# Kernel optimization log

Hardware: AMD Instinct MI355X
Metric: run time of the kernel (lower is better)

Reference implementation:

```python
import jax, jax.numpy as jnp
import numpy as np

EMB_DIM = 512
R_DIM = 64
B, S = 8, 2048


def _lowrank_params(key):
    k1, k2, k3, k4 = jax.random.split(key, 4)
    s1 = 1.0 / np.sqrt(EMB_DIM)
    s2 = 1.0 / np.sqrt(R_DIM)
    w1 = jax.random.uniform(k1, (EMB_DIM, R_DIM), jnp.float32, -s1, s1)
    b1 = jax.random.uniform(k2, (R_DIM,), jnp.float32, -s1, s1)
    w2 = jax.random.uniform(k3, (R_DIM, EMB_DIM), jnp.float32, -s2, s2)
    b2 = jax.random.uniform(k4, (EMB_DIM,), jnp.float32, -s2, s2)
    return w1, b1, w2, b2


def setup_inputs() -> dict:
    key = jax.random.key(0)
    kx, km, kq, kk, kv = jax.random.split(key, 5)
    x = jax.random.normal(kx, (B, S, EMB_DIM), jnp.float32)
    attention_mask = jax.random.randint(km, (B, S), 0, 2, jnp.int32)
    q_w1, q_b1, q_w2, q_b2 = _lowrank_params(kq)
    k_w1, k_b1, k_w2, k_b2 = _lowrank_params(kk)
    v_w1, v_b1, v_w2, v_b2 = _lowrank_params(kv)
    return dict(x=x, attention_mask=attention_mask,
                q_w1=q_w1, q_b1=q_b1, q_w2=q_w2, q_b2=q_b2,
                k_w1=k_w1, k_b1=k_b1, k_w2=k_w2, k_b2=k_b2,
                v_w1=v_w1, v_b1=v_b1, v_w2=v_w2, v_b2=v_b2)


def _proj(x, w1, b1, w2, b2):
    # low-rank projection: emb -> r -> emb (two stacked Linears, no nonlinearity)
    return (x @ w1 + b1) @ w2 + b2


def reference(x, attention_mask,
              q_w1, q_b1, q_w2, q_b2,
              k_w1, k_b1, k_w2, k_b2,
              v_w1, v_b1, v_w2, v_b2):
    q = _proj(x, q_w1, q_b1, q_w2, q_b2)   # [B,S,E]
    k = _proj(x, k_w1, k_b1, k_w2, k_b2)   # [B,S,E]
    v = _proj(x, v_w1, v_b1, v_w2, v_b2)   # [B,S,E]
    scale = EMB_DIM ** (-0.5)
    scores = jnp.einsum('bse,bte->bst', q, k) * scale  # [B,S,S]
    m = attention_mask.astype(jnp.float32)
    scores = scores * m[:, :, None] * m[:, None, :]
    temp = jnp.einsum('bst,bte->bse', scores, v)       # [B,S,E]
    out = jax.nn.softmax(temp, axis=-1)                # softmax AFTER second bmm (non-standard)
    return out, q
```

## Files before the change

kernel.cpp:

```cpp
#include <hip/hip_runtime.h>
#include <hip/hip_bf16.h>

#define SCALE 0.044194173824159216f

typedef float f32x4 __attribute__((ext_vector_type(4)));
typedef __bf16 bf16x8 __attribute__((ext_vector_type(8)));

static __device__ __forceinline__ unsigned short f2bf(float f){
  unsigned u = __builtin_bit_cast(unsigned, f);
  u += 0x7fffu + ((u >> 16) & 1u);
  return (unsigned short)(u >> 16);
}

__global__ __launch_bounds__(256) void kA(const float* __restrict__ w1q, const float* __restrict__ w1k,
    const float* __restrict__ w1v, const float* __restrict__ w2q, const float* __restrict__ b2q,
    const float* __restrict__ w2k, const float* __restrict__ b2k,
    unsigned short* __restrict__ W1T, unsigned short* __restrict__ W2qT, float* __restrict__ Pm){
  const int bid = blockIdx.x, t = threadIdx.x;
  if (bid < 64){
    #pragma unroll
    for (int s = 0; s < 8; s++){
      int id = s*16384 + bid*256 + t;
      if (id < 192*512){
        int n = id >> 9, k = id & 511;
        int p = n >> 6, c = n & 63;
        const float* w1 = (p==0)? w1q : ((p==1)? w1k : w1v);
        W1T[id] = f2bf(w1[k*64 + c]);
      } else {
        int j = id - 192*512;
        int e = j >> 6, r = j & 63;
        W2qT[j] = f2bf(w2q[r*512 + e]);
      }
    }
  } else {
    int id = (bid - 64)*256 + t;
    if (id >= 65*65) return;
    int i = id / 65, j = id - i*65;
    const float* qi = (i < 64)? (w2q + i*512) : b2q;
    const float* kj = (j < 64)? (w2k + j*512) : b2k;
    float s = 0.f;
    for (int e = 0; e < 512; e += 4){
      float4 a = *(const float4*)(qi + e);
      float4 b = *(const float4*)(kj + e);
      s += a.x*b.x; s += a.y*b.y; s += a.z*b.z; s += a.w*b.w;
    }
    Pm[id] = s * SCALE;
  }
}

__global__ __launch_bounds__(256) void kB(const float* __restrict__ x, const unsigned short* __restrict__ W1T,
    const float* __restrict__ b1q, const float* __restrict__ b1k, const float* __restrict__ b1v,
    const int* __restrict__ mask,
    unsigned short* __restrict__ Hq, float* __restrict__ part){
  __shared__ __attribute__((aligned(16))) char smem[33792];
  unsigned short (*Ax)[40] = (unsigned short(*)[40])smem;
  unsigned short (*Bt)[40] = (unsigned short(*)[40])(smem + 5120);
  float (*ak)[66] = (float(*)[66])smem;
  float (*av)[66] = (float(*)[66])(smem + 16896);
  const int t = threadIdx.x;
  const int lane = t & 63, wave = t >> 6;
  const int l15 = lane & 15, lg = lane >> 4, ks = lg * 8;
  const int r0 = blockIdx.x * 64;
  f32x4 acc[12];
  #pragma unroll
  for (int j = 0; j < 12; j++) acc[j] = (f32x4){0.f,0.f,0.f,0.f};
  for (int k0 = 0; k0 < 512; k0 += 32){
    #pragma unroll
    for (int s = 0; s < 2; s++){
      int i = t + 256*s;
      int r = i >> 3, kq = (i & 7) * 4;
      float4 v = *(const float4*)(x + (size_t)(r0 + r)*512 + k0 + kq);
      ushort4 pk; pk.x = f2bf(v.x); pk.y = f2bf(v.y); pk.z = f2bf(v.z); pk.w = f2bf(v.w);
      *(ushort4*)&Ax[r][kq] = pk;
    }
    #pragma unroll
    for (int s = 0; s < 3; s++){
      int i = t + 256*s;
      int n = i >> 2, kq = (i & 3) * 8;
      *(uint4*)&Bt[n][kq] = *(const uint4*)(W1T + n*512 + k0 + kq);
    }
    __syncthreads();
    const int arow = (wave << 4) | l15;
    bf16x8 af = *(const bf16x8*)&Ax[arow][ks];
    #pragma unroll
    for (int j = 0; j < 12; j++){
      bf16x8 bf = *(const bf16x8*)&Bt[j*16 + l15][ks];
      acc[j] = __builtin_amdgcn_mfma_f32_16x16x32_bf16(af, bf, acc[j], 0, 0, 0);
    }
    __syncthreads();
  }
  int rowl[4]; float mrow[4];
  #pragma unroll
  for (int rg = 0; rg < 4; rg++){
    rowl[rg] = (wave << 4) + (lg << 2) + rg;
    mrow[rg] = (float)mask[r0 + rowl[rg]];
  }
  #pragma unroll
  for (int j = 0; j < 4; j++){
    int c = (j << 4) | l15;
    float bias = b1q[c];
    #pragma unroll
    for (int rg = 0; rg < 4; rg++)
      Hq[(size_t)(r0 + rowl[rg])*64 + c] = f2bf(acc[j][rg] + bias);
  }
  #pragma unroll
  for (int j = 0; j < 4; j++){
    int c = (j << 4) | l15;
    float bias = b1k[c];
    #pragma unroll
    for (int rg = 0; rg < 4; rg++)
      ak[rowl[rg]][c] = (acc[4 + j][rg] + bias) * mrow[rg];
  }
  #pragma unroll
  for (int j = 0; j < 4; j++){
    int c = (j << 4) | l15;
    float bias = b1v[c];
    #pragma unroll
    for (int rg = 0; rg < 4; rg++)
      av[rowl[rg]][c] = acc[8 + j][rg] + bias;
  }
  if (t < 64){ ak[t][64] = (float)mask[r0 + t]; av[t][64] = 1.f; }
  __syncthreads();
  if (t < 169){
    int tj = t / 13, ti = t - tj*13;
    int i0 = ti * 5, j0 = tj * 5;
    float pacc[5][5];
    #pragma unroll
    for (int a = 0; a < 5; a++)
      #pragma unroll
      for (int v = 0; v < 5; v++) pacc[a][v] = 0.f;
    for (int r = 0; r < 64; r++){
      float a[5], v[5];
      #pragma unroll
      for (int ii = 0; ii < 5; ii++) a[ii] = ak[r][i0 + ii];
      #pragma unroll
      for (int jj = 0; jj < 5; jj++) v[jj] = av[r][j0 + jj];
      #pragma unroll
      for (int ii = 0; ii < 5; ii++)
        #pragma unroll
        for (int jj = 0; jj < 5; jj++) pacc[ii][jj] += a[ii] * v[jj];
    }
    float* pout = part + (size_t)blockIdx.x * 4225;
    #pragma unroll
    for (int ii = 0; ii < 5; ii++)
      #pragma unroll
      for (int jj = 0; jj < 5; jj++)
        pout[(i0 + ii)*65 + (j0 + jj)] = pacc[ii][jj];
  }
}

__global__ __launch_bounds__(256) void kR(const float* __restrict__ part, float* __restrict__ At){
  int g = blockIdx.x*256 + threadIdx.x;
  if (g < 33800){
    int b = g / 4225, e = g - b*4225;
    const float* p = part + (size_t)b*135200 + e;
    float s = 0.f;
    #pragma unroll
    for (int ch = 0; ch < 32; ch++) s += p[(size_t)ch*4225];
    At[g] = s;
  }
}

__global__ __launch_bounds__(256) void k3b(const float* __restrict__ At, const float* __restrict__ Pm,
    const float* __restrict__ w2v, const float* __restrict__ b2v,
    unsigned short* __restrict__ GtA, float* __restrict__ Gbias){
  __shared__ float Pl[65*66];
  __shared__ float Atl[65*66];
  __shared__ float T1l[65*66];
  const int t = threadIdx.x;
  const int b = blockIdx.x >> 3, ec = (blockIdx.x & 7) << 6;
  for (int id = t; id < 4225; id += 256){
    int i = id / 65, j = id - i*65;
    Pl[i*66 + j]  = Pm[id];
    Atl[i*66 + j] = At[(size_t)b*4225 + id];
  }
  __syncthreads();
  if (t < 169){
    int tj = t / 13, ti = t - tj*13;
    int i0 = ti * 5, j0 = tj * 5;
    float acc[5][5];
    #pragma unroll
    for (int a = 0; a < 5; a++)
      #pragma unroll
      for (int v = 0; v < 5; v++) acc[a][v] = 0.f;
    for (int k = 0; k < 65; k++){
      float a[5], vv[5];
      #pragma unroll
      for (int ii = 0; ii < 5; ii++) a[ii] = Pl[(i0 + ii)*66 + k];
      #pragma unroll
      for (int jj = 0; jj < 5; jj++) vv[jj] = Atl[k*66 + j0 + jj];
      #pragma unroll
      for (int ii = 0; ii < 5; ii++)
        #pragma unroll
        for (int jj = 0; jj < 5; jj++) acc[ii][jj] += a[ii] * vv[jj];
    }
    #pragma unroll
    for (int ii = 0; ii < 5; ii++)
      #pragma unroll
      for (int jj = 0; jj < 5; jj++) T1l[(i0 + ii)*66 + (j0 + jj)] = acc[ii][jj];
  }
  __syncthreads();
  for (int id = t; id < 4096; id += 256){
    int j = id >> 6, c = id & 63;
    Pl[j*66 + c] = w2v[j*512 + ec + c];
  }
  __syncthreads();
  if (t < 169){
    int tj = t / 13, ti = t - tj*13;
    int i0 = ti * 5, j0 = tj * 5;
    float acc[5][5];
    #pragma unroll
    for (int a = 0; a < 5; a++)
      #pragma unroll
      for (int v = 0; v < 5; v++) acc[a][v] = 0.f;
    for (int k = 0; k < 64; k++){
      float a[5], vv[5];
      #pragma unroll
      for (int ii = 0; ii < 5; ii++) a[ii] = T1l[(i0 + ii)*66 + k];
      #pragma unroll
      for (int jj = 0; jj < 5; jj++) vv[jj] = Pl[k*66 + j0 + jj];
      #pragma unroll
      for (int ii = 0; ii < 5; ii++)
        #pragma unroll
        for (int jj = 0; jj < 5; jj++) acc[ii][jj] += a[ii] * vv[jj];
    }
    #pragma unroll
    for (int ii = 0; ii < 5; ii++){
      int r = i0 + ii;
      float t64 = T1l[r*66 + 64];
      #pragma unroll
      for (int jj = 0; jj < 5; jj++){
        int ej = j0 + jj;
        if (ej < 64){
          int e = ec + ej;
          float s = acc[ii][jj] + t64 * b2v[e];
          if (r < 64) GtA[((size_t)b*512 + e)*64 + r] = f2bf(s);
          else        Gbias[b*512 + e] = s;
        }
      }
    }
  }
}

__global__ __launch_bounds__(256) void kD(const unsigned short* __restrict__ Hq, const unsigned short* __restrict__ W2qT,
    const unsigned short* __restrict__ GtA, const float* __restrict__ Gbias, const float* __restrict__ b2q,
    const int* __restrict__ mask, float* __restrict__ out, float* __restrict__ qout){
  const int t = threadIdx.x, lane = t & 63, wave = t >> 6;
  const int b = blockIdx.x >> 5, rc = (blockIdx.x & 31) << 6;
  const int l15 = lane & 15, lg = lane >> 4, ks = lg * 8;
  const size_t gr0 = (size_t)b*2048 + rc;
  const int arow = (wave << 4) | l15;
  const unsigned short* arp = Hq + (gr0 + arow)*64 + ks;
  bf16x8 a0 = *(const bf16x8*)arp;
  bf16x8 a1 = *(const bf16x8*)(arp + 32);
  const unsigned short* Bsrc = GtA + (size_t)b*512*64;
  f32x4 acc[32];
  #pragma unroll
  for (int f = 0; f < 32; f++) acc[f] = (f32x4){0.f,0.f,0.f,0.f};
  #pragma unroll
  for (int f = 0; f < 32; f++){
    int col = (f << 4) | l15;
    bf16x8 b0 = *(const bf16x8*)(Bsrc + col*64 + ks);
    bf16x8 b1 = *(const bf16x8*)(Bsrc + col*64 + 32 + ks);
    acc[f] = __builtin_amdgcn_mfma_f32_16x16x32_bf16(a0, b0, acc[f], 0, 0, 0);
    acc[f] = __builtin_amdgcn_mfma_f32_16x16x32_bf16(a1, b1, acc[f], 0, 0, 0);
  }
  #pragma unroll
  for (int f = 0; f < 32; f++){
    float gbv = Gbias[(b << 9) | (f << 4) | l15];
    #pragma unroll
    for (int rg = 0; rg < 4; rg++) acc[f][rg] += gbv;
  }
  #pragma unroll
  for (int rg = 0; rg < 4; rg++){
    int row = rc + (wave << 4) + (lg << 2) + rg;
    float m = (float)mask[b*2048 + row];
    float mx = -3.4e38f;
    #pragma unroll
    for (int f = 0; f < 32; f++){
      float v = acc[f][rg] * m;
      acc[f][rg] = v;
      mx = fmaxf(mx, v);
    }
    #pragma unroll
    for (int d = 1; d < 16; d <<= 1) mx = fmaxf(mx, __shfl_xor(mx, d, 64));
    float sum = 0.f;
    #pragma unroll
    for (int f = 0; f < 32; f++){
      float ev = __expf(acc[f][rg] - mx);
      acc[f][rg] = ev;
      sum += ev;
    }
    #pragma unroll
    for (int d = 1; d < 16; d <<= 1) sum += __shfl_xor(sum, d, 64);
    float inv = 1.f / sum;
    float* orow = out + ((size_t)b*2048 + row) * 512;
    #pragma unroll
    for (int f = 0; f < 32; f++) orow[(f << 4) | l15] = acc[f][rg] * inv;
  }
  #pragma unroll
  for (int f = 0; f < 32; f++) acc[f] = (f32x4){0.f,0.f,0.f,0.f};
  #pragma unroll
  for (int f = 0; f < 32; f++){
    int col = (f << 4) | l15;
    bf16x8 b0 = *(const bf16x8*)(W2qT + col*64 + ks);
    bf16x8 b1 = *(const bf16x8*)(W2qT + col*64 + 32 + ks);
    acc[f] = __builtin_amdgcn_mfma_f32_16x16x32_bf16(a0, b0, acc[f], 0, 0, 0);
    acc[f] = __builtin_amdgcn_mfma_f32_16x16x32_bf16(a1, b1, acc[f], 0, 0, 0);
  }
  #pragma unroll
  for (int f = 0; f < 32; f++){
    int col = (f << 4) | l15;
    float bias = b2q[col];
    #pragma unroll
    for (int rg = 0; rg < 4; rg++){
      int row = rc + (wave << 4) + (lg << 2) + rg;
      qout[((size_t)b*2048 + row) * 512 + col] = acc[f][rg] + bias;
    }
  }
}

extern "C" void kernel_launch(void* const* d_in, const int* in_sizes, int n_in,
                              void* d_out, int out_size, void* d_ws, size_t ws_size,
                              hipStream_t stream){
  const float* x    = (const float*)d_in[0];
  const int*   mask = (const int*)d_in[1];
  const float* q_w1 = (const float*)d_in[2];
  const float* q_b1 = (const float*)d_in[3];
  const float* q_w2 = (const float*)d_in[4];
  const float* q_b2 = (const float*)d_in[5];
  const float* k_w1 = (const float*)d_in[6];
  const float* k_b1 = (const float*)d_in[7];
  const float* k_w2 = (const float*)d_in[8];
  const float* k_b2 = (const float*)d_in[9];
  const float* v_w1 = (const float*)d_in[10];
  const float* v_b1 = (const float*)d_in[11];
  const float* v_w2 = (const float*)d_in[12];
  const float* v_b2 = (const float*)d_in[13];

  char* ws = (char*)d_ws;
  unsigned short* W1T  = (unsigned short*)(ws + 0);
  unsigned short* W2qT = (unsigned short*)(ws + 196608);
  float*          Pm   = (float*)(ws + 262144);
  unsigned short* Hq   = (unsigned short*)(ws + 279296);
  float*          part = (float*)(ws + 2376448);
  float*          At   = (float*)(ws + 6702848);
  unsigned short* GtA  = (unsigned short*)(ws + 6838272);
  float*          Gbias= (float*)(ws + 7362560);

  float* out  = (float*)d_out;
  float* qout = out + (size_t)8*2048*512;

  kA <<<81,  256, 0, stream>>>(q_w1, k_w1, v_w1, q_w2, q_b2, k_w2, k_b2, W1T, W2qT, Pm);
  kB <<<256, 256, 0, stream>>>(x, W1T, q_b1, k_b1, v_b1, mask, Hq, part);
  kR <<<133, 256, 0, stream>>>(part, At);
  k3b<<<64,  256, 0, stream>>>(At, Pm, v_w2, v_b2, GtA, Gbias);
  kD <<<256, 256, 0, stream>>>(Hq, W2qT, GtA, Gbias, q_b2, mask, out, qout);
}
```

Baseline: 89.96 us.

## Fuse five kernels into one persistent kernel with global atomic barriers

Merges the weight-prep, first projection, reduction, small-matrix, and final output kernels into a single launch of 256 blocks. The stages are separated by a grid-wide barrier built on an agent-scope atomic counter, which is zeroed by a memset before each launch. The aim is to remove the launch gaps and tail idle time between the five small stages. In exchange it relies on all 256 blocks being resident at once, and its spin loop has a timeout that could silently break the ordering between stages.

```diff
diff --git a/kernel.cpp b/kernel.cpp
--- a/kernel.cpp
+++ b/kernel.cpp
@@ -12,310 +12,330 @@
   return (unsigned short)(u >> 16);
 }
 
-__global__ __launch_bounds__(256) void kA(const float* __restrict__ w1q, const float* __restrict__ w1k,
-    const float* __restrict__ w1v, const float* __restrict__ w2q, const float* __restrict__ b2q,
+static __device__ __forceinline__ void gbar(unsigned* bar, int e){
+  __syncthreads();
+  if (threadIdx.x == 0){
+    __threadfence();
+    __hip_atomic_fetch_add(&bar[e], 1u, __ATOMIC_ACQ_REL, __HIP_MEMORY_SCOPE_AGENT);
+    unsigned spins = 0;
+    while (__hip_atomic_load(&bar[e], __ATOMIC_ACQUIRE, __HIP_MEMORY_SCOPE_AGENT) < 256u){
+      __builtin_amdgcn_s_sleep(2);
+      if (++spins > (1u << 22)) break;
+    }
+  }
+  __syncthreads();
+  __threadfence();
+}
+
+__global__ __launch_bounds__(256) void mha_fused(
+    const float* __restrict__ x, const int* __restrict__ mask,
+    const float* __restrict__ w1q, const float* __restrict__ b1q,
+    const float* __restrict__ w2q, const float* __restrict__ b2q,
+    const float* __restrict__ w1k, const float* __restrict__ b1k,
     const float* __restrict__ w2k, const float* __restrict__ b2k,
-    unsigned short* __restrict__ W1T, unsigned short* __restrict__ W2qT, float* __restrict__ Pm){
-  const int bid = blockIdx.x, t = threadIdx.x;
+    const float* __restrict__ w1v, const float* __restrict__ b1v,
+    const float* __restrict__ w2v, const float* __restrict__ b2v,
+    unsigned short* __restrict__ W1T, unsigned short* __restrict__ W2qT,
+    float* __restrict__ Pm, unsigned short* __restrict__ Hq,
+    float* __restrict__ part, float* __restrict__ At,
+    unsigned short* __restrict__ GtA, float* __restrict__ Gbias,
+    float* __restrict__ out, float* __restrict__ qout, unsigned* bar)
+{
+  __shared__ __attribute__((aligned(16))) char smem[51712];
+  const int t = threadIdx.x, bid = blockIdx.x;
+  const int lane = t & 63, wave = t >> 6;
+  const int l15 = lane & 15, lg = lane >> 4, ks = lg * 8;
+
   if (bid < 64){
     #pragma unroll
     for (int s = 0; s < 8; s++){
       int id = s*16384 + bid*256 + t;
-      if (id < 192*512){
+      if (id < 98304){
         int n = id >> 9, k = id & 511;
         int p = n >> 6, c = n & 63;
         const float* w1 = (p==0)? w1q : ((p==1)? w1k : w1v);
         W1T[id] = f2bf(w1[k*64 + c]);
       } else {
-        int j = id - 192*512;
+        int j = id - 98304;
         int e = j >> 6, r = j & 63;
         W2qT[j] = f2bf(w2q[r*512 + e]);
       }
     }
-  } else {
+  } else if (bid < 81){
     int id = (bid - 64)*256 + t;
-    if (id >= 65*65) return;
-    int i = id / 65, j = id - i*65;
-    const float* qi = (i < 64)? (w2q + i*512) : b2q;
-    const float* kj = (j < 64)? (w2k + j*512) : b2k;
-    float s = 0.f;
-    for (int e = 0; e < 512; e += 4){
-      float4 a = *(const float4*)(qi + e);
-      float4 b = *(const float4*)(kj + e);
-      s += a.x*b.x; s += a.y*b.y; s += a.z*b.z; s += a.w*b.w;
-    }
-    Pm[id] = s * SCALE;
-  }
-}
-
-__global__ __launch_bounds__(256) void kB(const float* __restrict__ x, const unsigned short* __restrict__ W1T,
-    const float* __restrict__ b1q, const float* __restrict__ b1k, const float* __restrict__ b1v,
-    const int* __restrict__ mask,
-    unsigned short* __restrict__ Hq, float* __restrict__ part){
-  __shared__ __attribute__((aligned(16))) char smem[33792];
-  unsigned short (*Ax)[40] = (unsigned short(*)[40])smem;
-  unsigned short (*Bt)[40] = (unsigned short(*)[40])(smem + 5120);
-  float (*ak)[66] = (float(*)[66])smem;
-  float (*av)[66] = (float(*)[66])(smem + 16896);
-  const int t = threadIdx.x;
-  const int lane = t & 63, wave = t >> 6;
-  const int l15 = lane & 15, lg = lane >> 4, ks = lg * 8;
-  const int r0 = blockIdx.x * 64;
-  f32x4 acc[12];
-  #pragma unroll
-  for (int j = 0; j < 12; j++) acc[j] = (f32x4){0.f,0.f,0.f,0.f};
-  for (int k0 = 0; k0 < 512; k0 += 32){
-    #pragma unroll
-    for (int s = 0; s < 2; s++){
-      int i = t + 256*s;
-      int r = i >> 3, kq = (i & 7) * 4;
-      float4 v = *(const float4*)(x + (size_t)(r0 + r)*512 + k0 + kq);
-      ushort4 pk; pk.x = f2bf(v.x); pk.y = f2bf(v.y); pk.z = f2bf(v.z); pk.w = f2bf(v.w);
-      *(ushort4*)&Ax[r][kq] = pk;
-    }
-    #pragma unroll
-    for (int s = 0; s < 3; s++){
-      int i = t + 256*s;
-      int n = i >> 2, kq = (i & 3) * 8;
-      *(uint4*)&Bt[n][kq] = *(const uint4*)(W1T + n*512 + k0 + kq);
-    }
+    if (id < 4225){
+      int i = id / 65, j = id - i*65;
+      const float* qi = (i < 64)? (w2q + i*512) : b2q;
+      const float* kj = (j < 64)? (w2k + j*512) : b2k;
+      float s = 0.f;
+      for (int e = 0; e < 512; e += 4){
+        float4 a = *(const float4*)(qi + e);
+        float4 b = *(const float4*)(kj + e);
+        s += a.x*b.x + a.y*b.y + a.z*b.z + a.w*b.w;
+      }
+      Pm[id] = s * SCALE;
+    }
+  }
+  gbar(bar, 0);
+
+  {
+    unsigned short (*Ax)[40] = (unsigned short(*)[40])smem;
+    unsigned short (*Bt)[40] = (unsigned short(*)[40])(smem + 5120);
+    float (*ak)[66] = (float(*)[66])smem;
+    float (*av)[66] = (float(*)[66])(smem + 16896);
+    const int r0 = bid * 64;
+    f32x4 acc[12];
+    #pragma unroll
+    for (int j = 0; j < 12; j++) acc[j] = (f32x4){0.f,0.f,0.f,0.f};
+    for (int k0 = 0; k0 < 512; k0 += 32){
+      #pragma unroll
+      for (int s = 0; s < 2; s++){
+        int i = t + 256*s;
+        int r = i >> 3, kq = (i & 7) * 4;
+        float4 v = *(const float4*)(x + (size_t)(r0 + r)*512 + k0 + kq);
+        ushort4 pk; pk.x = f2bf(v.x); pk.y = f2bf(v.y); pk.z = f2bf(v.z); pk.w = f2bf(v.w);
+        *(ushort4*)&Ax[r][kq] = pk;
+      }
+      #pragma unroll
+      for (int s = 0; s < 3; s++){
+        int i = t + 256*s;
+        int n = i >> 2, kq = (i & 3) * 8;
+        *(uint4*)&Bt[n][kq] = *(const uint4*)(W1T + n*512 + k0 + kq);
+      }
+      __syncthreads();
+      const int arow = (wave << 4) | l15;
+      bf16x8 af = *(const bf16x8*)&Ax[arow][ks];
+      #pragma unroll
+      for (int j = 0; j < 12; j++){
+        bf16x8 bf = *(const bf16x8*)&Bt[j*16 + l15][ks];
+        acc[j] = __builtin_amdgcn_mfma_f32_16x16x32_bf16(af, bf, acc[j], 0, 0, 0);
+      }
+      __syncthreads();
+    }
+    int rowl[4]; float mrow[4];
+    #pragma unroll
+    for (int rg = 0; rg < 4; rg++){
+      rowl[rg] = (wave << 4) + (lg << 2) + rg;
+      mrow[rg] = (float)mask[r0 + rowl[rg]];
+    }
+    #pragma unroll
+    for (int j = 0; j < 4; j++){
+      int c = (j << 4) | l15;
+      float bias = b1q[c];
+      #pragma unroll
+      for (int rg = 0; rg < 4; rg++)
+        Hq[(size_t)(r0 + rowl[rg])*64 + c] = f2bf(acc[j][rg] + bias);
+    }
+    #pragma unroll
+    for (int j = 0; j < 4; j++){
+      int c = (j << 4) | l15;
+      float bias = b1k[c];
+      #pragma unroll
+      for (int rg = 0; rg < 4; rg++)
+        ak[rowl[rg]][c] = (acc[4 + j][rg] + bias) * mrow[rg];
+    }
+    #pragma unroll
+    for (int j = 0; j < 4; j++){
+      int c = (j << 4) | l15;
+      float bias = b1v[c];
+      #pragma unroll
+      for (int rg = 0; rg < 4; rg++)
+        av[rowl[rg]][c] = acc[8 + j][rg] + bias;
+    }
+    if (t < 64){ ak[t][64] = (float)mask[r0 + t]; av[t][64] = 1.f; }
     __syncthreads();
+    if (t < 169){
+      int tj = t / 13, ti = t - tj*13;
+      int i0 = ti * 5, j0 = tj * 5;
+      float pacc[5][5];
+      #pragma unroll
+      for (int a = 0; a < 5; a++)
+        #pragma unroll
+        for (int v = 0; v < 5; v++) pacc[a][v] = 0.f;
+      for (int r = 0; r < 64; r++){
+        float a[5], v[5];
+        #pragma unroll
+        for (int ii = 0; ii < 5; ii++) a[ii] = ak[r][i0 + ii];
+        #pragma unroll
+        for (int jj = 0; jj < 5; jj++) v[jj] = av[r][j0 + jj];
+        #pragma unroll
+        for (int ii = 0; ii < 5; ii++)
+          #pragma unroll
+          for (int jj = 0; jj < 5; jj++) pacc[ii][jj] += a[ii] * v[jj];
+      }
+      float* pout = part + (size_t)bid * 4225;
+      #pragma unroll
+      for (int ii = 0; ii < 5; ii++)
+        #pragma unroll
+        for (int jj = 0; jj < 5; jj++)
+          pout[(i0 + ii)*65 + (j0 + jj)] = pacc[ii][jj];
+    }
+  }
+  gbar(bar, 1);
+
+  {
+    int g = bid*256 + t;
+    if (g < 33800){
+      int b = g / 4225, e = g - b*4225;
+      const float* p = part + (size_t)b*135200 + e;
+      float s = 0.f;
+      #pragma unroll
+      for (int ch = 0; ch < 32; ch++) s += p[(size_t)ch*4225];
+      At[g] = s;
+    }
+  }
+  gbar(bar, 2);
+
+  if (bid < 64){
+    float* Pl  = (float*)smem;
+    float* Atl = Pl + 4290;
+    float* T1l = Atl + 4290;
+    const int b = bid >> 3, ec = (bid & 7) << 6;
+    for (int id = t; id < 4225; id += 256){
+      int i = id / 65, j = id - i*65;
+      Pl[i*66 + j]  = Pm[id];
+      Atl[i*66 + j] = At[(size_t)b*4225 + id];
+    }
+    __syncthreads();
+    if (t < 169){
+      int tj = t / 13, ti = t - tj*13;
+      int i0 = ti * 5, j0 = tj * 5;
+      float acc[5][5];
+      #pragma unroll
+      for (int a = 0; a < 5; a++)
+        #pragma unroll
+        for (int v = 0; v < 5; v++) acc[a][v] = 0.f;
+      for (int k = 0; k < 65; k++){
+        float a[5], vv[5];
+        #pragma unroll
+        for (int ii = 0; ii < 5; ii++) a[ii] = Pl[(i0 + ii)*66 + k];
+        #pragma unroll
+        for (int jj = 0; jj < 5; jj++) vv[jj] = Atl[k*66 + j0 + jj];
+        #pragma unroll
+        for (int ii = 0; ii < 5; ii++)
+          #pragma unroll
+          for (int jj = 0; jj < 5; jj++) acc[ii][jj] += a[ii] * vv[jj];
+      }
+      #pragma unroll
+      for (int ii = 0; ii < 5; ii++)
+        #pragma unroll
+        for (int jj = 0; jj < 5; jj++) T1l[(i0 + ii)*66 + (j0 + jj)] = acc[ii][jj];
+    }
+    __syncthreads();
+    for (int id = t; id < 4096; id += 256){
+      int j = id >> 6, c = id & 63;
+      Pl[j*66 + c] = w2v[j*512 + ec + c];
+    }
+    __syncthreads();
+    if (t < 169){
+      int tj = t / 13, ti = t - tj*13;
+      int i0 = ti * 5, j0 = tj * 5;
+      float acc[5][5];
+      #pragma unroll
+      for (int a = 0; a < 5; a++)
+        #pragma unroll
+        for (int v = 0; v < 5; v++) acc[a][v] = 0.f;
+      for (int k = 0; k < 64; k++){
+        float a[5], vv[5];
+        #pragma unroll
+        for (int ii = 0; ii < 5; ii++) a[ii] = T1l[(i0 + ii)*66 + k];
+        #pragma unroll
+        for (int jj = 0; jj < 5; jj++) vv[jj] = Pl[k*66 + j0 + jj];
+        #pragma unroll
+        for (int ii = 0; ii < 5; ii++)
+          #pragma unroll
+          for (int jj = 0; jj < 5; jj++) acc[ii][jj] += a[ii] * vv[jj];
+      }
+      #pragma unroll
+      for (int ii = 0; ii < 5; ii++){
+        int r = i0 + ii;
+        float t64 = T1l[r*66 + 64];
+        #pragma unroll
+        for (int jj = 0; jj < 5; jj++){
+          int ej = j0 + jj;
+          if (ej < 64){
+            int e = ec + ej;
+            float s = acc[ii][jj] + t64 * b2v[e];
+            if (r < 64) GtA[((size_t)b*512 + e)*64 + r] = f2bf(s);
+            else        Gbias[b*512 + e] = s;
+          }
+        }
+      }
+    }
+  }
+  gbar(bar, 3);
+
+  {
+    const int b = bid >> 5, rc = (bid & 31) << 6;
+    const size_t gr0 = (size_t)b*2048 + rc;
     const int arow = (wave << 4) | l15;
-    bf16x8 af = *(const bf16x8*)&Ax[arow][ks];
-    #pragma unroll
-    for (int j = 0; j < 12; j++){
-      bf16x8 bf = *(const bf16x8*)&Bt[j*16 + l15][ks];
-      acc[j] = __builtin_amdgcn_mfma_f32_16x16x32_bf16(af, bf, acc[j], 0, 0, 0);
-    }
-    __syncthreads();
-  }
-  int rowl[4]; float mrow[4];
-  #pragma unroll
-  for (int rg = 0; rg < 4; rg++){
-    rowl[rg] = (wave << 4) + (lg << 2) + rg;
-    mrow[rg] = (float)mask[r0 + rowl[rg]];
-  }
-  #pragma unroll
-  for (int j = 0; j < 4; j++){
-    int c = (j << 4) | l15;
-    float bias = b1q[c];
-    #pragma unroll
-    for (int rg = 0; rg < 4; rg++)
-      Hq[(size_t)(r0 + rowl[rg])*64 + c] = f2bf(acc[j][rg] + bias);
-  }
-  #pragma unroll
-  for (int j = 0; j < 4; j++){
-    int c = (j << 4) | l15;
-    float bias = b1k[c];
-    #pragma unroll
-    for (int rg = 0; rg < 4; rg++)
-      ak[rowl[rg]][c] = (acc[4 + j][rg] + bias) * mrow[rg];
-  }
-  #pragma unroll
-  for (int j = 0; j < 4; j++){
-    int c = (j << 4) | l15;
-    float bias = b1v[c];
-    #pragma unroll
-    for (int rg = 0; rg < 4; rg++)
-      av[rowl[rg]][c] = acc[8 + j][rg] + bias;
-  }
-  if (t < 64){ ak[t][64] = (float)mask[r0 + t]; av[t][64] = 1.f; }
-  __syncthreads();
-  if (t < 169){
-    int tj = t / 13, ti = t - tj*13;
-    int i0 = ti * 5, j0 = tj * 5;
-    float pacc[5][5];
-    #pragma unroll
-    for (int a = 0; a < 5; a++)
-      #pragma unroll
-      for (int v = 0; v < 5; v++) pacc[a][v] = 0.f;
-    for (int r = 0; r < 64; r++){
-      float a[5], v[5];
-      #pragma unroll
-      for (int ii = 0; ii < 5; ii++) a[ii] = ak[r][i0 + ii];
-      #pragma unroll
-      for (int jj = 0; jj < 5; jj++) v[jj] = av[r][j0 + jj];
-      #pragma unroll
-      for (int ii = 0; ii < 5; ii++)
-        #pragma unroll
-        for (int jj = 0; jj < 5; jj++) pacc[ii][jj] += a[ii] * v[jj];
-    }
-    float* pout = part + (size_t)blockIdx.x * 4225;
-    #pragma unroll
-    for (int ii = 0; ii < 5; ii++)
-      #pragma unroll
-      for (int jj = 0; jj < 5; jj++)
-        pout[(i0 + ii)*65 + (j0 + jj)] = pacc[ii][jj];
-  }
-}
-
-__global__ __launch_bounds__(256) void kR(const float* __restrict__ part, float* __restrict__ At){
-  int g = blockIdx.x*256 + threadIdx.x;
-  if (g < 33800){
-    int b = g / 4225, e = g - b*4225;
-    const float* p = part + (size_t)b*135200 + e;
-    float s = 0.f;
-    #pragma unroll
-    for (int ch = 0; ch < 32; ch++) s += p[(size_t)ch*4225];
-    At[g] = s;
-  }
-}
-
-__global__ __launch_bounds__(256) void k3b(const float* __restrict__ At, const float* __restrict__ Pm,
-    const float* __restrict__ w2v, const float* __restrict__ b2v,
-    unsigned short* __restrict__ GtA, float* __restrict__ Gbias){
-  __shared__ float Pl[65*66];
-  __shared__ float Atl[65*66];
-  __shared__ float T1l[65*66];
-  const int t = threadIdx.x;
-  const int b = blockIdx.x >> 3, ec = (blockIdx.x & 7) << 6;
-  for (int id = t; id < 4225; id += 256){
-    int i = id / 65, j = id - i*65;
-    Pl[i*66 + j]  = Pm[id];
-    Atl[i*66 + j] = At[(size_t)b*4225 + id];
-  }
-  __syncthreads();
-  if (t < 169){
-    int tj = t / 13, ti = t - tj*13;
-    int i0 = ti * 5, j0 = tj * 5;
-    float acc[5][5];
-    #pragma unroll
-    for (int a = 0; a < 5; a++)
-      #pragma unroll
-      for (int v = 0; v < 5; v++) acc[a][v] = 0.f;
-    for (int k = 0; k < 65; k++){
-      float a[5], vv[5];
-      #pragma unroll
-      for (int ii = 0; ii < 5; ii++) a[ii] = Pl[(i0 + ii)*66 + k];
-      #pragma unroll
-      for (int jj = 0; jj < 5; jj++) vv[jj] = Atl[k*66 + j0 + jj];
-      #pragma unroll
-      for (int ii = 0; ii < 5; ii++)
-        #pragma unroll
-        for (int jj = 0; jj < 5; jj++) acc[ii][jj] += a[ii] * vv[jj];
-    }
-    #pragma unroll
-    for (int ii = 0; ii < 5; ii++)
-      #pragma unroll
-      for (int jj = 0; jj < 5; jj++) T1l[(i0 + ii)*66 + (j0 + jj)] = acc[ii][jj];
-  }
-  __syncthreads();
-  for (int id = t; id < 4096; id += 256){
-    int j = id >> 6, c = id & 63;
-    Pl[j*66 + c] = w2v[j*512 + ec + c];
-  }
-  __syncthreads();
-  if (t < 169){
-    int tj = t / 13, ti = t - tj*13;
-    int i0 = ti * 5, j0 = tj * 5;
-    float acc[5][5];
-    #pragma unroll
-    for (int a = 0; a < 5; a++)
-      #pragma unroll
-      for (int v = 0; v < 5; v++) acc[a][v] = 0.f;
-    for (int k = 0; k < 64; k++){
-      float a[5], vv[5];
-      #pragma unroll
-      for (int ii = 0; ii < 5; ii++) a[ii] = T1l[(i0 + ii)*66 + k];
-      #pragma unroll
-      for (int jj = 0; jj < 5; jj++) vv[jj] = Pl[k*66 + j0 + jj];
-      #pragma unroll
-      for (int ii = 0; ii < 5; ii++)
-        #pragma unroll
-        for (int jj = 0; jj < 5; jj++) acc[ii][jj] += a[ii] * vv[jj];
-    }
-    #pragma unroll
-    for (int ii = 0; ii < 5; ii++){
-      int r = i0 + ii;
-      float t64 = T1l[r*66 + 64];
-      #pragma unroll
-      for (int jj = 0; jj < 5; jj++){
-        int ej = j0 + jj;
-        if (ej < 64){
-          int e = ec + ej;
-          float s = acc[ii][jj] + t64 * b2v[e];
-          if (r < 64) GtA[((size_t)b*512 + e)*64 + r] = f2bf(s);
-          else        Gbias[b*512 + e] = s;
-        }
-      }
-    }
-  }
-}
-
-__global__ __launch_bounds__(256) void kD(const unsigned short* __restrict__ Hq, const unsigned short* __restrict__ W2qT,
-    const unsigned short* __restrict__ GtA, const float* __restrict__ Gbias, const float* __restrict__ b2q,
-    const int* __restrict__ mask, float* __restrict__ out, float* __restrict__ qout){
-  const int t = threadIdx.x, lane = t & 63, wave = t >> 6;
-  const int b = blockIdx.x >> 5, rc = (blockIdx.x & 31) << 6;
-  const int l15 = lane & 15, lg = lane >> 4, ks = lg * 8;
-  const size_t gr0 = (size_t)b*2048 + rc;
-  const int arow = (wave << 4) | l15;
-  const unsigned short* arp = Hq + (gr0 + arow)*64 + ks;
-  bf16x8 a0 = *(const bf16x8*)arp;
-  bf16x8 a1 = *(const bf16x8*)(arp + 32);
-  const unsigned short* Bsrc = GtA + (size_t)b*512*64;
-  f32x4 acc[32];
-  #pragma unroll
-  for (int f = 0; f < 32; f++) acc[f] = (f32x4){0.f,0.f,0.f,0.f};
-  #pragma unroll
-  for (int f = 0; f < 32; f++){
-    int col = (f << 4) | l15;
-    bf16x8 b0 = *(const bf16x8*)(Bsrc + col*64 + ks);
-    bf16x8 b1 = *(const bf16x8*)(Bsrc + col*64 + 32 + ks);
-    acc[f] = __builtin_amdgcn_mfma_f32_16x16x32_bf16(a0, b0, acc[f], 0, 0, 0);
-    acc[f] = __builtin_amdgcn_mfma_f32_16x16x32_bf16(a1, b1, acc[f], 0, 0, 0);
-  }
-  #pragma unroll
-  for (int f = 0; f < 32; f++){
-    float gbv = Gbias[(b << 9) | (f << 4) | l15];
-    #pragma unroll
-    for (int rg = 0; rg < 4; rg++) acc[f][rg] += gbv;
-  }
-  #pragma unroll
-  for (int rg = 0; rg < 4; rg++){
-    int row = rc + (wave << 4) + (lg << 2) + rg;
-    float m = (float)mask[b*2048 + row];
-    float mx = -3.4e38f;
+    const unsigned short* arp = Hq + (gr0 + arow)*64 + ks;
+    bf16x8 a0 = *(const bf16x8*)arp;
+    bf16x8 a1 = *(const bf16x8*)(arp + 32);
+    const unsigned short* Bsrc = GtA + (size_t)b*512*64;
+    f32x4 acc[32];
+    #pragma unroll
+    for (int f = 0; f < 32; f++) acc[f] = (f32x4){0.f,0.f,0.f,0.f};
     #pragma unroll
     for (int f = 0; f < 32; f++){
-      float v = acc[f][rg] * m;
-      acc[f][rg] = v;
-      mx = fmaxf(mx, v);
-    }
-    #pragma unroll
-    for (int d = 1; d < 16; d <<= 1) mx = fmaxf(mx, __shfl_xor(mx, d, 64));
-    float sum = 0.f;
+      int col = (f << 4) | l15;
+      bf16x8 b0 = *(const bf16x8*)(Bsrc + col*64 + ks);
+      bf16x8 b1 = *(const bf16x8*)(Bsrc + col*64 + 32 + ks);
+      acc[f] = __builtin_amdgcn_mfma_f32_16x16x32_bf16(a0, b0, acc[f], 0, 0, 0);
+      acc[f] = __builtin_amdgcn_mfma_f32_16x16x32_bf16(a1, b1, acc[f], 0, 0, 0);
+    }
     #pragma unroll
     for (int f = 0; f < 32; f++){
-      float ev = __expf(acc[f][rg] - mx);
-      acc[f][rg] = ev;
-      sum += ev;
-    }
-    #pragma unroll
-    for (int d = 1; d < 16; d <<= 1) sum += __shfl_xor(sum, d, 64);
-    float inv = 1.f / sum;
-    float* orow = out + ((size_t)b*2048 + row) * 512;
-    #pragma unroll
-    for (int f = 0; f < 32; f++) orow[(f << 4) | l15] = acc[f][rg] * inv;
-  }
-  #pragma unroll
-  for (int f = 0; f < 32; f++) acc[f] = (f32x4){0.f,0.f,0.f,0.f};
-  #pragma unroll
-  for (int f = 0; f < 32; f++){
-    int col = (f << 4) | l15;
-    bf16x8 b0 = *(const bf16x8*)(W2qT + col*64 + ks);
-    bf16x8 b1 = *(const bf16x8*)(W2qT + col*64 + 32 + ks);
-    acc[f] = __builtin_amdgcn_mfma_f32_16x16x32_bf16(a0, b0, acc[f], 0, 0, 0);
-    acc[f] = __builtin_amdgcn_mfma_f32_16x16x32_bf16(a1, b1, acc[f], 0, 0, 0);
-  }
-  #pragma unroll
-  for (int f = 0; f < 32; f++){
-    int col = (f << 4) | l15;
-    float bias = b2q[col];
+      float gbv = Gbias[(b << 9) | (f << 4) | l15];
+      #pragma unroll
+      for (int rg = 0; rg < 4; rg++) acc[f][rg] += gbv;
+    }
     #pragma unroll
     for (int rg = 0; rg < 4; rg++){
       int row = rc + (wave << 4) + (lg << 2) + rg;
-      qout[((size_t)b*2048 + row) * 512 + col] = acc[f][rg] + bias;
+      float m = (float)mask[b*2048 + row];
+      float mx = -3.4e38f;
+      #pragma unroll
+      for (int f = 0; f < 32; f++){
+        float v = acc[f][rg] * m;
+        acc[f][rg] = v;
+        mx = fmaxf(mx, v);
+      }
+      #pragma unroll
+      for (int d = 1; d < 16; d <<= 1) mx = fmaxf(mx, __shfl_xor(mx, d, 64));
+      float sum = 0.f;
+      #pragma unroll
+      for (int f = 0; f < 32; f++){
+        float ev = __expf(acc[f][rg] - mx);
+        acc[f][rg] = ev;
+        sum += ev;
+      }
+      #pragma unroll
+      for (int d = 1; d < 16; d <<= 1) sum += __shfl_xor(sum, d, 64);
+      float inv = 1.f / sum;
+      float* orow = out + ((size_t)b*2048 + row) * 512;
+      #pragma unroll
+      for (int f = 0; f < 32; f++) orow[(f << 4) | l15] = acc[f][rg] * inv;
+    }
+    #pragma unroll
+    for (int f = 0; f < 32; f++) acc[f] = (f32x4){0.f,0.f,0.f,0.f};
+    #pragma unroll
+    for (int f = 0; f < 32; f++){
+      int col = (f << 4) | l15;
+      bf16x8 b0 = *(const bf16x8*)(W2qT + col*64 + ks);
+      bf16x8 b1 = *(const bf16x8*)(W2qT + col*64 + 32 + ks);
+      acc[f] = __builtin_amdgcn_mfma_f32_16x16x32_bf16(a0, b0, acc[f], 0, 0, 0);
+      acc[f] = __builtin_amdgcn_mfma_f32_16x16x32_bf16(a1, b1, acc[f], 0, 0, 0);
+    }
+    #pragma unroll
+    for (int f = 0; f < 32; f++){
+      int col = (f << 4) | l15;
+      float bias = b2q[col];
+      #pragma unroll
+      for (int rg = 0; rg < 4; rg++){
+        int row = rc + (wave << 4) + (lg << 2) + rg;
+        qout[((size_t)b*2048 + row) * 512 + col] = acc[f][rg] + bias;
+      }
     }
   }
 }
@@ -347,13 +367,13 @@
   float*          At   = (float*)(ws + 6702848);
   unsigned short* GtA  = (unsigned short*)(ws + 6838272);
   float*          Gbias= (float*)(ws + 7362560);
+  unsigned*       bar  = (unsigned*)(ws + 7378944);
 
   float* out  = (float*)d_out;
   float* qout = out + (size_t)8*2048*512;
 
-  kA <<<81,  256, 0, stream>>>(q_w1, k_w1, v_w1, q_w2, q_b2, k_w2, k_b2, W1T, W2qT, Pm);
-  kB <<<256, 256, 0, stream>>>(x, W1T, q_b1, k_b1, v_b1, mask, Hq, part);
-  kR <<<133, 256, 0, stream>>>(part, At);
-  k3b<<<64,  256, 0, stream>>>(At, Pm, v_w2, v_b2, GtA, Gbias);
-  kD <<<256, 256, 0, stream>>>(Hq, W2qT, GtA, Gbias, q_b2, mask, out, qout);
+  hipMemsetAsync(bar, 0, 4*sizeof(unsigned), stream);
+  mha_fused<<<256, 256, 0, stream>>>(x, mask,
+      q_w1, q_b1, q_w2, q_b2, k_w1, k_b1, k_w2, k_b2, v_w1, v_b1, v_w2, v_b2,
+      W1T, W2qT, Pm, Hq, part, At, GtA, Gbias, out, qout, bar);
 }
```

After: 279.1 us. 210% more time.
